# Kernel tuning notes

Hardware: AMD Instinct MI355X
Metric: run time of the kernel (lower is better)

The kernel has to match this reference:

```python
import jax, jax.numpy as jnp
import numpy as np

B, D, HID, DC, K = 32768, 64, 512, 128, 12
CLAMP = 1.0
L1 = D // 2          # GLOW split lengths
L2 = D - L1
INIT = 0.01          # torch code rescales all params to 0.01*randn


def setup_inputs() -> dict:
    key = jax.random.key(0)
    ks = iter(jax.random.split(key, 16))
    # FrEIA PermuteRandom: np.random.seed(k); np.random.permutation(D)
    perms = jnp.asarray(
        np.stack([np.random.RandomState(k).permutation(D) for k in range(K)]),
        dtype=jnp.int32)
    f32 = jnp.float32
    return {
        'q_feat': jax.random.normal(next(ks), (B, 1, D), f32),
        'H': jax.random.normal(next(ks), (B, DC), f32),
        'perms': perms,
        'an_logscale': INIT * jax.random.normal(next(ks), (K, D), f32),
        'an_bias': INIT * jax.random.normal(next(ks), (K, D), f32),
        's1_W1': INIT * jax.random.normal(next(ks), (K, HID, L1 + DC), f32),
        's1_b1': INIT * jax.random.normal(next(ks), (K, HID), f32),
        's1_W2': INIT * jax.random.normal(next(ks), (K, 2 * L2, HID), f32),
        's1_b2': INIT * jax.random.normal(next(ks), (K, 2 * L2), f32),
        's2_W1': INIT * jax.random.normal(next(ks), (K, HID, L2 + DC), f32),
        's2_b1': INIT * jax.random.normal(next(ks), (K, HID), f32),
        's2_W2': INIT * jax.random.normal(next(ks), (K, 2 * L1, HID), f32),
        's2_b2': INIT * jax.random.normal(next(ks), (K, 2 * L1), f32),
    }


def _mlp(x, W1, b1, W2, b2):
    # torch Linear: y = x @ W.T + b
    h = jax.nn.relu(x @ W1.T + b1)
    return h @ W2.T + b2


def _log_e(s):
    # FrEIA GLOW soft clamp: log e(s) = clamp * 0.636 * atan(s / clamp)
    return CLAMP * 0.636 * jnp.arctan(s / CLAMP)


def reference(q_feat, H, perms, an_logscale, an_bias,
              s1_W1, s1_b1, s1_W2, s1_b2,
              s2_W1, s2_b1, s2_W2, s2_b2):
    x = q_feat.reshape(q_feat.shape[0], -1)          # Flatten: (B,1,D)->(B,D)
    logj = jnp.zeros(x.shape[0], x.dtype)

    def block(carry, p):
        x, logj = carry
        perm, ls, bi, w11, b11, w12, b12, w21, b21, w22, b22 = p
        x = x[:, perm]                               # PermuteRandom (logdet 0)
        x = x * jnp.exp(ls) + bi                     # ActNorm
        logj = logj + jnp.sum(ls)
        x1, x2 = x[:, :L1], x[:, L1:]                # GLOW coupling
        r2 = _mlp(jnp.concatenate([x2, H], 1), w21, b21, w22, b22)
        le2 = _log_e(r2[:, :L1])
        y1 = jnp.exp(le2) * x1 + r2[:, L1:]
        r1 = _mlp(jnp.concatenate([y1, H], 1), w11, b11, w12, b12)
        le1 = _log_e(r1[:, :L2])
        y2 = jnp.exp(le1) * x2 + r1[:, L2:]
        logj = logj + jnp.sum(le1, axis=1) + jnp.sum(le2, axis=1)
        return (jnp.concatenate([y1, y2], 1), logj), None

    (z, logj), _ = jax.lax.scan(
        block, (x, logj),
        (perms, an_logscale, an_bias,
         s1_W1, s1_b1, s1_W2, s1_b2,
         s2_W1, s2_b1, s2_W2, s2_b2))
    return z, logj
```

## Files before the change

### kernel.cpp

```cpp
#include <hip/hip_runtime.h>
#include <hip/hip_bf16.h>
#include <math.h>

#define B_ROWS 32768

typedef __attribute__((ext_vector_type(8)))  short        s8v;
typedef __attribute__((ext_vector_type(4)))  float        f4v;
typedef __attribute__((ext_vector_type(2)))  unsigned int u2v;
typedef __attribute__((ext_vector_type(4)))  unsigned int u4v;

__device__ __forceinline__ short f2bf(float f){
  unsigned u = __builtin_bit_cast(unsigned, f);
  u = (u + 0x7fffu + ((u >> 16) & 1u)) >> 16;
  return (short)u;
}
__device__ __forceinline__ unsigned cpk(float a, float b){
  __hip_bfloat16_raw lo = (__hip_bfloat16_raw)__float2bfloat16(a);
  __hip_bfloat16_raw hi = (__hip_bfloat16_raw)__float2bfloat16(b);
  return (unsigned)lo.x | ((unsigned)hi.x << 16);
}
__device__ __forceinline__ float bf_lo(unsigned u){ return __builtin_bit_cast(float, u << 16); }
__device__ __forceinline__ float bf_hi(unsigned u){ return __builtin_bit_cast(float, u & 0xffff0000u); }

__device__ __forceinline__ float atan_f(float t){
  float a = fabsf(t);
  bool big = a > 1.0f;
  float u = big ? __builtin_amdgcn_rcpf(t) : t;
  float s = u * u;
  float p = fmaf(fmaf(fmaf(fmaf(s, 0.0208351f, -0.0851330f), s, 0.1801410f), s, -0.3302995f), s, 0.9998660f);
  p = u * p;
  float base = __builtin_copysignf(1.57079633f, t);
  return big ? base - p : p;
}

#define MFMA16(A,B,C) __builtin_amdgcn_mfma_f32_16x16x32_bf16((A),(B),(C),0,0,0)

typedef __attribute__((address_space(1))) const unsigned int gu32;
typedef __attribute__((address_space(3))) unsigned int lu32;
__device__ __forceinline__ void gl_lds16(const unsigned short* g, char* l){
  __builtin_amdgcn_global_load_lds((gu32*)(const void*)g, (lu32*)(void*)l, 16, 0, 0);
}

#define OXFT 0
#define XFT_S 68
#define OXHB 17408
#define XHB_S 40
#define OHB  22528
#define HB_S 72
#define OSL  31744
#define SL_S 68
#define OW1  40448
#define W1BUF 20480
#define OLJ  81408
#define SM_SZ 81664

#define WF_W2 1966080
#define W_TOTAL 2752512

__global__ void cvtw_frag(const float* __restrict__ s1w1, const float* __restrict__ s1w2,
                          const float* __restrict__ s2w1, const float* __restrict__ s2w2,
                          unsigned short* __restrict__ dst)
{
  long t = (long)blockIdx.x * blockDim.x + threadIdx.x;
  if (t >= W_TOTAL) return;
  float v;
  if (t < WF_W2){
    int m = (int)(t / 81920); int r = (int)(t - (long)m*81920);
    int c = r / 10240;  int r2 = r - c*10240;
    int tile = r2 >> 9; int r3 = r2 & 511;
    int lane = r3 >> 3; int e = r3 & 7;
    int rg = tile / 5,  kk = tile - rg*5;
    int l15 = lane & 15, lq = lane >> 4;
    int h  = c*64 + rg*16 + l15;
    int ki = kk*32 + lq*8 + e;
    const float* src = (m & 1) ? s1w1 : s2w1;
    v = src[(size_t)(m >> 1)*81920 + h*160 + ki];
  } else {
    long u = t - WF_W2;
    int m = (int)(u / 32768); int r = (int)(u - (long)m*32768);
    int g = r >> 9; int r3 = r & 511;
    int lane = r3 >> 3; int e = r3 & 7;
    int c = g >> 3, hs = (g >> 2) & 1, ot = g & 3;
    int l15 = lane & 15, lq = lane >> 4;
    int o = ot*16 + l15;
    int h = c*64 + hs*32 + lq*8 + e;
    const float* src = (m & 1) ? s1w2 : s2w2;
    v = src[(size_t)(m >> 1)*32768 + o*512 + h];
  }
  dst[t] = (unsigned short)f2bf(v);
}

__global__ __launch_bounds__(256, 2) void cinn_dma2(
    const float* __restrict__ q, const float* __restrict__ Hg,
    const int* __restrict__ perms,
    const float* __restrict__ ls_g, const float* __restrict__ bi_g,
    const float* __restrict__ s1b1, const float* __restrict__ s1b2,
    const float* __restrict__ s2b1, const float* __restrict__ s2b2,
    const unsigned short* __restrict__ wbf,
    float* __restrict__ outz, float* __restrict__ outlj)
{
  __shared__ __align__(16) char sm[SM_SZ];
  const int tid = threadIdx.x;
  const int rowbase = blockIdx.x * 64;
  const int lane = tid & 63, wave = tid >> 6;
  const int hw = wave >> 1, ng = wave & 1;
  const int l15 = lane & 15, lq = lane >> 4;

  float* XFT = (float*)(sm + OXFT);
  short* XHB = (short*)(sm + OXHB);
  short* HB  = (short*)(sm + OHB);
  float* LOGJ= (float*)(sm + OLJ);

  {
    int b = tid >> 2, j = tid & 3;
    const float* src = q + (size_t)(rowbase + b)*64 + j*16;
    #pragma unroll
    for (int i = 0; i < 4; ++i){
      f4v v = *(const f4v*)(src + 4*i);
      #pragma unroll
      for (int jj = 0; jj < 4; ++jj)
        XFT[(j*16 + 4*i + jj)*XFT_S + b] = v[jj];
    }
  }
  if (tid < 64) LOGJ[tid] = 0.f;
  __syncthreads();

  s8v hfr[2][4];
  #pragma unroll
  for (int nt = 0; nt < 2; ++nt){
    int b = rowbase + ng*32 + nt*16 + l15;
    #pragma unroll
    for (int kkh = 0; kkh < 4; ++kkh){
      const float* hp = Hg + (size_t)b*128 + kkh*32 + lq*8;
      f4v a = *(const f4v*)hp;
      f4v c = *(const f4v*)(hp + 4);
      u4v u = {cpk(a[0],a[1]), cpk(a[2],a[3]), cpk(c[0],c[1]), cpk(c[2],c[3])};
      hfr[nt][kkh] = __builtin_bit_cast(s8v, u);
    }
  }

  {
    const unsigned short* g = wbf + wave*2560 + lane*8;
    char* lb = sm + OW1 + wave*5120;
    #pragma unroll
    for (int k = 0; k < 5; ++k) gl_lds16(g + k*512, lb + k*1024);
  }

  for (int m = 0; m < 24; ++m){
    const int bp = m & 1;
    const unsigned short* w1sec = wbf + (size_t)m*81920;
    const unsigned short* w2sec = wbf + WF_W2 + (size_t)m*32768;
    const float* b1p = (bp ? s1b1 : s2b1) + (m >> 1)*512;
    const float* b2p = (bp ? s1b2 : s2b2) + (m >> 1)*64;

    if (!bp){
      int blk = m >> 1;
      int   pd = perms[blk*64 + lane];
      float e  = __expf(ls_g[blk*64 + lane]);
      float bi = bi_g[blk*64 + lane];
      int bg = wave;
      f4v v[4];
      #pragma unroll
      for (int i = 0; i < 4; ++i)
        v[i] = *(const f4v*)(XFT + pd*XFT_S + bg*16 + 4*i);
      __syncthreads();
      #pragma unroll
      for (int i = 0; i < 4; ++i){
        #pragma unroll
        for (int jj = 0; jj < 4; ++jj) v[i][jj] = fmaf(v[i][jj], e, bi);
        *(f4v*)(XFT + lane*XFT_S + bg*16 + 4*i) = v[i];
      }
      if (lane >= 32){
        #pragma unroll
        for (int i = 0; i < 4; ++i)
          #pragma unroll
          for (int jj = 0; jj < 4; ++jj)
            XHB[(bg*16 + 4*i + jj)*XHB_S + (lane - 32)] = f2bf(v[i][jj]);
      }
      __syncthreads();
    }

    s8v xk[2];
    #pragma unroll
    for (int nt = 0; nt < 2; ++nt)
      xk[nt] = *(const s8v*)(XHB + (ng*32 + nt*16 + l15)*XHB_S + lq*8);

    f4v b2v[4];
    if (hw == 0){
      #pragma unroll
      for (int ot = 0; ot < 4; ++ot)
        b2v[ot] = *(const f4v*)(b2p + ot*16 + lq*4);
    }

    f4v racc[4][2];
    #pragma unroll
    for (int ot = 0; ot < 4; ++ot)
      #pragma unroll
      for (int nt = 0; nt < 2; ++nt)
        racc[ot][nt] = (f4v){0.f,0.f,0.f,0.f};

    #pragma unroll
    for (int c = 0; c < 8; ++c){
      if (!(m == 23 && c == 7)){
        const unsigned short* gsec = (c < 7) ? w1sec : (w1sec + 81920);
        const int cn = (c < 7) ? c + 1 : 0;
        const unsigned short* g = gsec + cn*10240 + wave*2560 + lane*8;
        char* lb = sm + OW1 + ((c+1)&1)*W1BUF + wave*5120;
        #pragma unroll
        for (int k = 0; k < 5; ++k) gl_lds16(g + k*512, lb + k*1024);
      }
      s8v w2c[4];
      #pragma unroll
      for (int ot = 0; ot < 4; ++ot)
        w2c[ot] = *(const s8v*)(w2sec + (size_t)((c*2 + hw)*4 + ot)*512 + lane*8);
      f4v b1v0 = *(const f4v*)(b1p + c*64 + hw*32 + lq*4);
      f4v b1v1 = *(const f4v*)(b1p + c*64 + hw*32 + 16 + lq*4);

      const short* W1c = (const short*)(sm + OW1 + (c&1)*W1BUF);
      f4v acc[2][2];
      #pragma unroll
      for (int mt = 0; mt < 2; ++mt)
        #pragma unroll
        for (int nt = 0; nt < 2; ++nt) acc[mt][nt] = (f4v){0.f,0.f,0.f,0.f};
      #pragma unroll
      for (int kk = 0; kk < 5; ++kk){
        s8v a0 = *(const s8v*)(W1c + ((hw*2 + 0)*5 + kk)*512 + lane*8);
        s8v a1 = *(const s8v*)(W1c + ((hw*2 + 1)*5 + kk)*512 + lane*8);
        #pragma unroll
        for (int nt = 0; nt < 2; ++nt){
          s8v bb = (kk == 0) ? xk[nt] : hfr[nt][kk-1];
          acc[0][nt] = MFMA16(a0, bb, acc[0][nt]);
          acc[1][nt] = MFMA16(a1, bb, acc[1][nt]);
        }
      }
      #pragma unroll
      for (int mt = 0; mt < 2; ++mt){
        f4v bv = mt ? b1v1 : b1v0;
        #pragma unroll
        for (int nt = 0; nt < 2; ++nt){
          float h0 = fmaxf(acc[mt][nt][0] + bv[0], 0.f);
          float h1 = fmaxf(acc[mt][nt][1] + bv[1], 0.f);
          float h2 = fmaxf(acc[mt][nt][2] + bv[2], 0.f);
          float h3 = fmaxf(acc[mt][nt][3] + bv[3], 0.f);
          *(u2v*)(HB + (ng*32 + nt*16 + l15)*HB_S + hw*32 + mt*16 + lq*4) = (u2v){cpk(h0,h1), cpk(h2,h3)};
        }
      }
      #pragma unroll
      for (int nt = 0; nt < 2; ++nt){
        s8v bb = *(const s8v*)(HB + (ng*32 + nt*16 + l15)*HB_S + hw*32 + lq*8);
        #pragma unroll
        for (int ot = 0; ot < 4; ++ot)
          racc[ot][nt] = MFMA16(w2c[ot], bb, racc[ot][nt]);
      }
      __syncthreads();
    }

    {
      short* SL = (hw == 0) ? (short*)(sm + OSL) : (short*)(sm + OHB);
      #pragma unroll
      for (int ot = 0; ot < 4; ++ot)
        #pragma unroll
        for (int nt = 0; nt < 2; ++nt){
          float r0 = racc[ot][nt][0], r1 = racc[ot][nt][1];
          float r2 = racc[ot][nt][2], r3 = racc[ot][nt][3];
          if (hw == 0){ r0 += b2v[ot][0]; r1 += b2v[ot][1]; r2 += b2v[ot][2]; r3 += b2v[ot][3]; }
          *(u2v*)(SL + (ng*32 + nt*16 + l15)*SL_S + ot*16 + lq*4) = (u2v){cpk(r0,r1), cpk(r2,r3)};
        }
    }
    __syncthreads();

    {
      int b = tid & 63, og = tid >> 6;
      float le[8] = {0,0,0,0,0,0,0,0}, ra[8] = {0,0,0,0,0,0,0,0};
      #pragma unroll
      for (int ms = 0; ms < 2; ++ms){
        const short* SL = (ms == 0) ? (const short*)(sm + OSL) : (const short*)(sm + OHB);
        u2v L0 = *(const u2v*)(SL + b*SL_S + og*8);
        u2v L1 = *(const u2v*)(SL + b*SL_S + og*8 + 4);
        u2v R0 = *(const u2v*)(SL + b*SL_S + 32 + og*8);
        u2v R1 = *(const u2v*)(SL + b*SL_S + 32 + og*8 + 4);
        le[0]+=bf_lo(L0[0]); le[1]+=bf_hi(L0[0]); le[2]+=bf_lo(L0[1]); le[3]+=bf_hi(L0[1]);
        le[4]+=bf_lo(L1[0]); le[5]+=bf_hi(L1[0]); le[6]+=bf_lo(L1[1]); le[7]+=bf_hi(L1[1]);
        ra[0]+=bf_lo(R0[0]); ra[1]+=bf_hi(R0[0]); ra[2]+=bf_lo(R0[1]); ra[3]+=bf_hi(R0[1]);
        ra[4]+=bf_lo(R1[0]); ra[5]+=bf_hi(R1[0]); ra[6]+=bf_lo(R1[1]); ra[7]+=bf_hi(R1[1]);
      }
      float part = 0.f, y[8];
      #pragma unroll
      for (int j = 0; j < 8; ++j){
        float l = 0.636f * atan_f(le[j]);
        int d = bp*32 + og*8 + j;
        y[j] = __expf(l) * XFT[d*XFT_S + b] + ra[j];
        XFT[d*XFT_S + b] = y[j];
        part += l;
      }
      if (!bp){
        u4v u = {cpk(y[0],y[1]), cpk(y[2],y[3]), cpk(y[4],y[5]), cpk(y[6],y[7])};
        *(u4v*)(XHB + b*XHB_S + og*8) = u;
      }
      atomicAdd(&LOGJ[b], part);
    }
    __syncthreads();
  }

  {
    int b = tid >> 2, j = tid & 3;
    float* dst = outz + (size_t)(rowbase + b)*64 + j*16;
    #pragma unroll
    for (int i = 0; i < 4; ++i){
      f4v w;
      #pragma unroll
      for (int jj = 0; jj < 4; ++jj)
        w[jj] = XFT[(j*16 + 4*i + jj)*XFT_S + b];
      *(f4v*)(dst + 4*i) = w;
    }
  }
  if (tid < 64){
    float p = 0.f;
    #pragma unroll
    for (int k = 0; k < 12; ++k) p += ls_g[k*64 + tid];
    #pragma unroll
    for (int off = 1; off < 64; off <<= 1) p += __shfl_xor(p, off);
    outlj[rowbase + tid] = LOGJ[tid] + p;
  }
}

extern "C" void kernel_launch(void* const* d_in, const int* in_sizes, int n_in,
                              void* d_out, int out_size, void* d_ws, size_t ws_size,
                              hipStream_t stream)
{
  const float* q    = (const float*)d_in[0];
  const float* Hg   = (const float*)d_in[1];
  const int*   perms= (const int*)  d_in[2];
  const float* ls   = (const float*)d_in[3];
  const float* bi   = (const float*)d_in[4];
  const float* s1W1 = (const float*)d_in[5];
  const float* s1b1 = (const float*)d_in[6];
  const float* s1W2 = (const float*)d_in[7];
  const float* s1b2 = (const float*)d_in[8];
  const float* s2W1 = (const float*)d_in[9];
  const float* s2b1 = (const float*)d_in[10];
  const float* s2W2 = (const float*)d_in[11];
  const float* s2b2 = (const float*)d_in[12];
  float* outz  = (float*)d_out;
  float* outlj = outz + (size_t)B_ROWS * 64;

  unsigned short* wbf = (unsigned short*)d_ws;
  cvtw_frag<<<2688, 1024, 0, stream>>>(s1W1, s1W2, s2W1, s2W2, wbf);
  cinn_dma2<<<512, 256, 0, stream>>>(q, Hg, perms, ls, bi,
                                     s1b1, s1b2, s2b1, s2b2,
                                     wbf, outz, outlj);
}
```

Baseline: 273.1 us.

## Widen blocks to 16 waves over 128 rows with larger W1 chunks

The fused flow kernel moves from 256-thread blocks on 64 rows to 1024-thread blocks on 128 rows. Each W1 chunk now covers 128 hidden units (40 KB, double-buffered), and the second-layer partial sums are split four ways across hidden-unit quarters. The aim is to have each weight chunk streamed into LDS serve twice as many rows, halving weight traffic per row and the number of chunk iterations. In exchange, LDS use grows to about 160 KB per block, so only one block fits per CU (256 blocks total). The four-way partial-sum reduction also adds LDS traffic and reuses the spare W1 buffer as scratch.

```diff
diff --git a/kernel.cpp b/kernel.cpp
--- a/kernel.cpp
+++ b/kernel.cpp
@@ -42,17 +42,17 @@
 }
 
 #define OXFT 0
-#define XFT_S 68
-#define OXHB 17408
+#define XFT_S 132
+#define OXHB 33792
 #define XHB_S 40
-#define OHB  22528
-#define HB_S 72
-#define OSL  31744
+#define OHB  44032
+#define HB_S 136
+#define OW1  78848
+#define W1BUF 40960
+#define OLJ  160768
+#define SM_SZ 161280
 #define SL_S 68
-#define OW1  40448
-#define W1BUF 20480
-#define OLJ  81408
-#define SM_SZ 81664
+#define SLOT_B 17408
 
 #define WF_W2 1966080
 #define W_TOTAL 2752512
@@ -66,12 +66,12 @@
   float v;
   if (t < WF_W2){
     int m = (int)(t / 81920); int r = (int)(t - (long)m*81920);
-    int c = r / 10240;  int r2 = r - c*10240;
+    int c = r / 20480;  int r2 = r - c*20480;
     int tile = r2 >> 9; int r3 = r2 & 511;
     int lane = r3 >> 3; int e = r3 & 7;
     int rg = tile / 5,  kk = tile - rg*5;
     int l15 = lane & 15, lq = lane >> 4;
-    int h  = c*64 + rg*16 + l15;
+    int h  = c*128 + rg*16 + l15;
     int ki = kk*32 + lq*8 + e;
     const float* src = (m & 1) ? s1w1 : s2w1;
     v = src[(size_t)(m >> 1)*81920 + h*160 + ki];
@@ -80,17 +80,24 @@
     int m = (int)(u / 32768); int r = (int)(u - (long)m*32768);
     int g = r >> 9; int r3 = r & 511;
     int lane = r3 >> 3; int e = r3 & 7;
-    int c = g >> 3, hs = (g >> 2) & 1, ot = g & 3;
+    int c = g >> 4, hw = (g >> 2) & 3, ot = g & 3;
     int l15 = lane & 15, lq = lane >> 4;
     int o = ot*16 + l15;
-    int h = c*64 + hs*32 + lq*8 + e;
+    int h = c*128 + hw*32 + lq*8 + e;
     const float* src = (m & 1) ? s1w2 : s2w2;
     v = src[(size_t)(m >> 1)*32768 + o*512 + h];
   }
   dst[t] = (unsigned short)f2bf(v);
 }
 
-__global__ __launch_bounds__(256, 2) void cinn_dma2(
+__device__ __forceinline__ void dma_w1(const unsigned short* gsec, char* lb, int wave, int lane){
+  gl_lds16(gsec + (size_t)wave*512 + lane*8,        lb + wave*1024);
+  gl_lds16(gsec + (size_t)(wave+16)*512 + lane*8,   lb + (wave+16)*1024);
+  if (wave < 8)
+    gl_lds16(gsec + (size_t)(wave+32)*512 + lane*8, lb + (wave+32)*1024);
+}
+
+__global__ __launch_bounds__(1024, 4) void cinn_w16(
     const float* __restrict__ q, const float* __restrict__ Hg,
     const int* __restrict__ perms,
     const float* __restrict__ ls_g, const float* __restrict__ bi_g,
@@ -101,9 +108,9 @@
 {
   __shared__ __align__(16) char sm[SM_SZ];
   const int tid = threadIdx.x;
-  const int rowbase = blockIdx.x * 64;
+  const int rowbase = blockIdx.x * 128;
   const int lane = tid & 63, wave = tid >> 6;
-  const int hw = wave >> 1, ng = wave & 1;
+  const int ng = wave >> 2, hw = wave & 3;
   const int l15 = lane & 15, lq = lane >> 4;
 
   float* XFT = (float*)(sm + OXFT);
@@ -112,17 +119,17 @@
   float* LOGJ= (float*)(sm + OLJ);
 
   {
-    int b = tid >> 2, j = tid & 3;
-    const float* src = q + (size_t)(rowbase + b)*64 + j*16;
-    #pragma unroll
-    for (int i = 0; i < 4; ++i){
-      f4v v = *(const f4v*)(src + 4*i);
-      #pragma unroll
-      for (int jj = 0; jj < 4; ++jj)
-        XFT[(j*16 + 4*i + jj)*XFT_S + b] = v[jj];
-    }
-  }
-  if (tid < 64) LOGJ[tid] = 0.f;
+    int b = tid >> 3, j = tid & 7;
+    const float* src = q + (size_t)(rowbase + b)*64 + j*8;
+    f4v v0 = *(const f4v*)src;
+    f4v v1 = *(const f4v*)(src + 4);
+    #pragma unroll
+    for (int jj = 0; jj < 4; ++jj){
+      XFT[(j*8 + jj)*XFT_S + b]     = v0[jj];
+      XFT[(j*8 + 4 + jj)*XFT_S + b] = v1[jj];
+    }
+  }
+  if (tid < 128) LOGJ[tid] = 0.f;
   __syncthreads();
 
   s8v hfr[2][4];
@@ -139,12 +146,7 @@
     }
   }
 
-  {
-    const unsigned short* g = wbf + wave*2560 + lane*8;
-    char* lb = sm + OW1 + wave*5120;
-    #pragma unroll
-    for (int k = 0; k < 5; ++k) gl_lds16(g + k*512, lb + k*1024);
-  }
+  dma_w1(wbf, sm + OW1, wave, lane);
 
   for (int m = 0; m < 24; ++m){
     const int bp = m & 1;
@@ -159,23 +161,23 @@
       float e  = __expf(ls_g[blk*64 + lane]);
       float bi = bi_g[blk*64 + lane];
       int bg = wave;
-      f4v v[4];
-      #pragma unroll
-      for (int i = 0; i < 4; ++i)
-        v[i] = *(const f4v*)(XFT + pd*XFT_S + bg*16 + 4*i);
+      f4v v[2];
+      #pragma unroll
+      for (int i = 0; i < 2; ++i)
+        v[i] = *(const f4v*)(XFT + pd*XFT_S + bg*8 + 4*i);
       __syncthreads();
       #pragma unroll
-      for (int i = 0; i < 4; ++i){
+      for (int i = 0; i < 2; ++i){
         #pragma unroll
         for (int jj = 0; jj < 4; ++jj) v[i][jj] = fmaf(v[i][jj], e, bi);
-        *(f4v*)(XFT + lane*XFT_S + bg*16 + 4*i) = v[i];
+        *(f4v*)(XFT + lane*XFT_S + bg*8 + 4*i) = v[i];
       }
       if (lane >= 32){
         #pragma unroll
-        for (int i = 0; i < 4; ++i)
+        for (int i = 0; i < 2; ++i)
           #pragma unroll
           for (int jj = 0; jj < 4; ++jj)
-            XHB[(bg*16 + 4*i + jj)*XHB_S + (lane - 32)] = f2bf(v[i][jj]);
+            XHB[(bg*8 + 4*i + jj)*XHB_S + (lane - 32)] = f2bf(v[i][jj]);
       }
       __syncthreads();
     }
@@ -200,21 +202,17 @@
         racc[ot][nt] = (f4v){0.f,0.f,0.f,0.f};
 
     #pragma unroll
-    for (int c = 0; c < 8; ++c){
-      if (!(m == 23 && c == 7)){
-        const unsigned short* gsec = (c < 7) ? w1sec : (w1sec + 81920);
-        const int cn = (c < 7) ? c + 1 : 0;
-        const unsigned short* g = gsec + cn*10240 + wave*2560 + lane*8;
-        char* lb = sm + OW1 + ((c+1)&1)*W1BUF + wave*5120;
-        #pragma unroll
-        for (int k = 0; k < 5; ++k) gl_lds16(g + k*512, lb + k*1024);
+    for (int c = 0; c < 4; ++c){
+      if (!(m == 23 && c == 3)){
+        const unsigned short* gsec = (c < 3) ? (w1sec + (c+1)*20480) : (w1sec + 81920);
+        dma_w1(gsec, sm + OW1 + ((c+1)&1)*W1BUF, wave, lane);
       }
       s8v w2c[4];
       #pragma unroll
       for (int ot = 0; ot < 4; ++ot)
-        w2c[ot] = *(const s8v*)(w2sec + (size_t)((c*2 + hw)*4 + ot)*512 + lane*8);
-      f4v b1v0 = *(const f4v*)(b1p + c*64 + hw*32 + lq*4);
-      f4v b1v1 = *(const f4v*)(b1p + c*64 + hw*32 + 16 + lq*4);
+        w2c[ot] = *(const s8v*)(w2sec + (size_t)((c*4 + hw)*4 + ot)*512 + lane*8);
+      f4v b1v0 = *(const f4v*)(b1p + c*128 + hw*32 + lq*4);
+      f4v b1v1 = *(const f4v*)(b1p + c*128 + hw*32 + 16 + lq*4);
 
       const short* W1c = (const short*)(sm + OW1 + (c&1)*W1BUF);
       f4v acc[2][2];
@@ -256,7 +254,8 @@
     }
 
     {
-      short* SL = (hw == 0) ? (short*)(sm + OSL) : (short*)(sm + OHB);
+      short* SL = (hw < 2) ? (short*)(sm + OHB + hw*SLOT_B)
+                           : (short*)(sm + OW1 + W1BUF + (hw-2)*SLOT_B);
       #pragma unroll
       for (int ot = 0; ot < 4; ++ot)
         #pragma unroll
@@ -270,54 +269,49 @@
     __syncthreads();
 
     {
-      int b = tid & 63, og = tid >> 6;
-      float le[8] = {0,0,0,0,0,0,0,0}, ra[8] = {0,0,0,0,0,0,0,0};
-      #pragma unroll
-      for (int ms = 0; ms < 2; ++ms){
-        const short* SL = (ms == 0) ? (const short*)(sm + OSL) : (const short*)(sm + OHB);
-        u2v L0 = *(const u2v*)(SL + b*SL_S + og*8);
-        u2v L1 = *(const u2v*)(SL + b*SL_S + og*8 + 4);
-        u2v R0 = *(const u2v*)(SL + b*SL_S + 32 + og*8);
-        u2v R1 = *(const u2v*)(SL + b*SL_S + 32 + og*8 + 4);
-        le[0]+=bf_lo(L0[0]); le[1]+=bf_hi(L0[0]); le[2]+=bf_lo(L0[1]); le[3]+=bf_hi(L0[1]);
-        le[4]+=bf_lo(L1[0]); le[5]+=bf_hi(L1[0]); le[6]+=bf_lo(L1[1]); le[7]+=bf_hi(L1[1]);
-        ra[0]+=bf_lo(R0[0]); ra[1]+=bf_hi(R0[0]); ra[2]+=bf_lo(R0[1]); ra[3]+=bf_hi(R0[1]);
-        ra[4]+=bf_lo(R1[0]); ra[5]+=bf_hi(R1[0]); ra[6]+=bf_lo(R1[1]); ra[7]+=bf_hi(R1[1]);
-      }
-      float part = 0.f, y[8];
-      #pragma unroll
-      for (int j = 0; j < 8; ++j){
+      int b = tid & 127, dg = tid >> 7;
+      float le[4] = {0,0,0,0}, ra[4] = {0,0,0,0};
+      #pragma unroll
+      for (int ms = 0; ms < 4; ++ms){
+        const short* SL = (ms < 2) ? (const short*)(sm + OHB + ms*SLOT_B)
+                                   : (const short*)(sm + OW1 + W1BUF + (ms-2)*SLOT_B);
+        u2v L = *(const u2v*)(SL + b*SL_S + dg*4);
+        u2v R = *(const u2v*)(SL + b*SL_S + 32 + dg*4);
+        le[0]+=bf_lo(L[0]); le[1]+=bf_hi(L[0]); le[2]+=bf_lo(L[1]); le[3]+=bf_hi(L[1]);
+        ra[0]+=bf_lo(R[0]); ra[1]+=bf_hi(R[0]); ra[2]+=bf_lo(R[1]); ra[3]+=bf_hi(R[1]);
+      }
+      float part = 0.f, y[4];
+      #pragma unroll
+      for (int j = 0; j < 4; ++j){
         float l = 0.636f * atan_f(le[j]);
-        int d = bp*32 + og*8 + j;
+        int d = bp*32 + dg*4 + j;
         y[j] = __expf(l) * XFT[d*XFT_S + b] + ra[j];
         XFT[d*XFT_S + b] = y[j];
         part += l;
       }
-      if (!bp){
-        u4v u = {cpk(y[0],y[1]), cpk(y[2],y[3]), cpk(y[4],y[5]), cpk(y[6],y[7])};
-        *(u4v*)(XHB + b*XHB_S + og*8) = u;
-      }
+      if (!bp)
+        *(u2v*)(XHB + b*XHB_S + dg*4) = (u2v){cpk(y[0],y[1]), cpk(y[2],y[3])};
       atomicAdd(&LOGJ[b], part);
     }
     __syncthreads();
   }
 
   {
-    int b = tid >> 2, j = tid & 3;
-    float* dst = outz + (size_t)(rowbase + b)*64 + j*16;
-    #pragma unroll
-    for (int i = 0; i < 4; ++i){
-      f4v w;
-      #pragma unroll
-      for (int jj = 0; jj < 4; ++jj)
-        w[jj] = XFT[(j*16 + 4*i + jj)*XFT_S + b];
-      *(f4v*)(dst + 4*i) = w;
-    }
-  }
-  if (tid < 64){
+    int b = tid >> 3, j = tid & 7;
+    float* dst = outz + (size_t)(rowbase + b)*64 + j*8;
+    f4v w0, w1;
+    #pragma unroll
+    for (int jj = 0; jj < 4; ++jj){
+      w0[jj] = XFT[(j*8 + jj)*XFT_S + b];
+      w1[jj] = XFT[(j*8 + 4 + jj)*XFT_S + b];
+    }
+    *(f4v*)dst = w0;
+    *(f4v*)(dst + 4) = w1;
+  }
+  if (tid < 128){
     float p = 0.f;
     #pragma unroll
-    for (int k = 0; k < 12; ++k) p += ls_g[k*64 + tid];
+    for (int k = 0; k < 12; ++k) p += ls_g[k*64 + lane];
     #pragma unroll
     for (int off = 1; off < 64; off <<= 1) p += __shfl_xor(p, off);
     outlj[rowbase + tid] = LOGJ[tid] + p;
@@ -346,7 +340,7 @@
 
   unsigned short* wbf = (unsigned short*)d_ws;
   cvtw_frag<<<2688, 1024, 0, stream>>>(s1W1, s1W2, s2W1, s2W2, wbf);
-  cinn_dma2<<<512, 256, 0, stream>>>(q, Hg, perms, ls, bi,
+  cinn_w16<<<256, 1024, 0, stream>>>(q, Hg, perms, ls, bi,
                                      s1b1, s1b2, s2b1, s2b2,
                                      wbf, outz, outlj);
 }
```

Result: slower. 484.0 us (+77.2%).

## Double row tile to 128 per block with 512 threads and wider hidden chunks

Applied to the files above, without the earlier changes.

The main kernel now handles 128 rows per block with 8 waves and 1 block per CU instead of 64 rows with 4 waves. Hidden units are processed in 4 chunks of 128, so each weight tile staged into LDS is reused across twice as many rows and the per-row weight traffic roughly halves. Bias adds are folded into the accumulator initialisation. The weight conversion kernel is rewritten to read 8 contiguous floats per thread and store packed 16-byte values in the same fragment layout. LDS use roughly doubles to about 160KB, so only one block fits per CU, which risks less latency hiding and only 256 blocks on the grid.

```diff
diff --git a/kernel.cpp b/kernel.cpp
--- a/kernel.cpp
+++ b/kernel.cpp
@@ -42,55 +42,55 @@
 }
 
 #define OXFT 0
-#define XFT_S 68
-#define OXHB 17408
+#define XFT_S 132
+#define OXHB 33792
 #define XHB_S 40
-#define OHB  22528
-#define HB_S 72
-#define OSL  31744
+#define OHB  44032
+#define HB_S 136
+#define OW1  78848
+#define W1BUF 40960
+#define OLJ  160768
+#define SM_SZ 161280
 #define SL_S 68
-#define OW1  40448
-#define W1BUF 20480
-#define OLJ  81408
-#define SM_SZ 81664
+#define SLOT_B 17408
 
 #define WF_W2 1966080
 #define W_TOTAL 2752512
 
-__global__ void cvtw_frag(const float* __restrict__ s1w1, const float* __restrict__ s1w2,
-                          const float* __restrict__ s2w1, const float* __restrict__ s2w2,
-                          unsigned short* __restrict__ dst)
+#define NT_W1 245760
+#define NT_W2 98304
+__global__ void cvtw_lin(const float* __restrict__ s1w1, const float* __restrict__ s1w2,
+                         const float* __restrict__ s2w1, const float* __restrict__ s2w2,
+                         unsigned short* __restrict__ dst)
 {
-  long t = (long)blockIdx.x * blockDim.x + threadIdx.x;
-  if (t >= W_TOTAL) return;
-  float v;
-  if (t < WF_W2){
-    int m = (int)(t / 81920); int r = (int)(t - (long)m*81920);
-    int c = r / 10240;  int r2 = r - c*10240;
-    int tile = r2 >> 9; int r3 = r2 & 511;
-    int lane = r3 >> 3; int e = r3 & 7;
-    int rg = tile / 5,  kk = tile - rg*5;
-    int l15 = lane & 15, lq = lane >> 4;
-    int h  = c*64 + rg*16 + l15;
-    int ki = kk*32 + lq*8 + e;
-    const float* src = (m & 1) ? s1w1 : s2w1;
-    v = src[(size_t)(m >> 1)*81920 + h*160 + ki];
-  } else {
-    long u = t - WF_W2;
-    int m = (int)(u / 32768); int r = (int)(u - (long)m*32768);
-    int g = r >> 9; int r3 = r & 511;
-    int lane = r3 >> 3; int e = r3 & 7;
-    int c = g >> 3, hs = (g >> 2) & 1, ot = g & 3;
-    int l15 = lane & 15, lq = lane >> 4;
-    int o = ot*16 + l15;
-    int h = c*64 + hs*32 + lq*8 + e;
-    const float* src = (m & 1) ? s1w2 : s2w2;
-    v = src[(size_t)(m >> 1)*32768 + o*512 + h];
-  }
-  dst[t] = (unsigned short)f2bf(v);
-}
-
-__global__ __launch_bounds__(256, 2) void cinn_dma2(
+  int t = blockIdx.x * blockDim.x + threadIdx.x;
+  if (t < NT_W1){
+    int lqkk = t % 20;  int u2 = t / 20;
+    int h = u2 & 127;   int mc = u2 >> 7;
+    int c = mc & 3,  m = mc >> 2;
+    int kk = lqkk >> 2, lq = lqkk & 3;
+    int rg = h >> 4, l15 = h & 15;
+    const float* src = ((m & 1) ? s1w1 : s2w1) + (size_t)(m >> 1)*81920
+                       + (size_t)(c*128 + h)*160 + lqkk*8;
+    f4v a = *(const f4v*)src;
+    f4v b = *(const f4v*)(src + 4);
+    u4v o = {cpk(a[0],a[1]), cpk(a[2],a[3]), cpk(b[0],b[1]), cpk(b[2],b[3])};
+    *(u4v*)(dst + (size_t)m*81920 + c*20480 + (rg*5 + kk)*512 + (lq*16 + l15)*8) = o;
+  } else if (t < NT_W1 + NT_W2){
+    int v = t - NT_W1;
+    int chl = v & 63;  int u2 = v >> 6;
+    int ol = u2 & 63;  int m = u2 >> 6;
+    int c = chl >> 4, hw = (chl >> 2) & 3, lq = chl & 3;
+    int ot = ol >> 4, l15 = ol & 15;
+    const float* src = ((m & 1) ? s1w2 : s2w2) + (size_t)(m >> 1)*32768 + (ot*16 + l15)*512 + chl*8;
+    f4v a = *(const f4v*)src;
+    f4v b = *(const f4v*)(src + 4);
+    u4v o = {cpk(a[0],a[1]), cpk(a[2],a[3]), cpk(b[0],b[1]), cpk(b[2],b[3])};
+    *(u4v*)(dst + WF_W2 + (size_t)m*32768 + ((c*4 + hw)*4 + ot)*512 + (lq*16 + l15)*8) = o;
+  }
+}
+
+__global__ __launch_bounds__(512, 1) void cinn_dma(
     const float* __restrict__ q, const float* __restrict__ Hg,
     const int* __restrict__ perms,
     const float* __restrict__ ls_g, const float* __restrict__ bi_g,
@@ -101,7 +101,7 @@
 {
   __shared__ __align__(16) char sm[SM_SZ];
   const int tid = threadIdx.x;
-  const int rowbase = blockIdx.x * 64;
+  const int rowbase = blockIdx.x * 128;
   const int lane = tid & 63, wave = tid >> 6;
   const int hw = wave >> 1, ng = wave & 1;
   const int l15 = lane & 15, lq = lane >> 4;
@@ -122,13 +122,13 @@
         XFT[(j*16 + 4*i + jj)*XFT_S + b] = v[jj];
     }
   }
-  if (tid < 64) LOGJ[tid] = 0.f;
+  if (tid < 128) LOGJ[tid] = 0.f;
   __syncthreads();
 
-  s8v hfr[2][4];
+  s8v hfr[4][4];
   #pragma unroll
-  for (int nt = 0; nt < 2; ++nt){
-    int b = rowbase + ng*32 + nt*16 + l15;
+  for (int nt = 0; nt < 4; ++nt){
+    int b = rowbase + ng*64 + nt*16 + l15;
     #pragma unroll
     for (int kkh = 0; kkh < 4; ++kkh){
       const float* hp = Hg + (size_t)b*128 + kkh*32 + lq*8;
@@ -180,74 +180,66 @@
       __syncthreads();
     }
 
-    s8v xk[2];
-    #pragma unroll
-    for (int nt = 0; nt < 2; ++nt)
-      xk[nt] = *(const s8v*)(XHB + (ng*32 + nt*16 + l15)*XHB_S + lq*8);
-
-    f4v b2v[4];
-    if (hw == 0){
+    s8v xk[4];
+    #pragma unroll
+    for (int nt = 0; nt < 4; ++nt)
+      xk[nt] = *(const s8v*)(XHB + (ng*64 + nt*16 + l15)*XHB_S + lq*8);
+
+    f4v racc[4][4];
+    #pragma unroll
+    for (int ot = 0; ot < 4; ++ot){
+      f4v bv = (f4v){0.f,0.f,0.f,0.f};
+      if (hw == 0) bv = *(const f4v*)(b2p + ot*16 + lq*4);
+      #pragma unroll
+      for (int nt = 0; nt < 4; ++nt) racc[ot][nt] = bv;
+    }
+
+    #pragma unroll
+    for (int c = 0; c < 4; ++c){
+      if (!(m == 23 && c == 3)){
+        const unsigned short* gsec = (c < 3) ? (w1sec + (c+1)*20480) : (w1sec + 81920);
+        const unsigned short* g = gsec + wave*2560 + lane*8;
+        char* lb = sm + OW1 + ((c+1)&1)*W1BUF + wave*5120;
+        #pragma unroll
+        for (int k = 0; k < 5; ++k) gl_lds16(g + k*512, lb + k*1024);
+      }
+      s8v w2c[4];
       #pragma unroll
       for (int ot = 0; ot < 4; ++ot)
-        b2v[ot] = *(const f4v*)(b2p + ot*16 + lq*4);
-    }
-
-    f4v racc[4][2];
-    #pragma unroll
-    for (int ot = 0; ot < 4; ++ot)
-      #pragma unroll
-      for (int nt = 0; nt < 2; ++nt)
-        racc[ot][nt] = (f4v){0.f,0.f,0.f,0.f};
-
-    #pragma unroll
-    for (int c = 0; c < 8; ++c){
-      if (!(m == 23 && c == 7)){
-        const unsigned short* gsec = (c < 7) ? w1sec : (w1sec + 81920);
-        const int cn = (c < 7) ? c + 1 : 0;
-        const unsigned short* g = gsec + cn*10240 + wave*2560 + lane*8;
-        char* lb = sm + OW1 + ((c+1)&1)*W1BUF + wave*5120;
-        #pragma unroll
-        for (int k = 0; k < 5; ++k) gl_lds16(g + k*512, lb + k*1024);
-      }
-      s8v w2c[4];
-      #pragma unroll
-      for (int ot = 0; ot < 4; ++ot)
-        w2c[ot] = *(const s8v*)(w2sec + (size_t)((c*2 + hw)*4 + ot)*512 + lane*8);
-      f4v b1v0 = *(const f4v*)(b1p + c*64 + hw*32 + lq*4);
-      f4v b1v1 = *(const f4v*)(b1p + c*64 + hw*32 + 16 + lq*4);
+        w2c[ot] = *(const s8v*)(w2sec + (size_t)((c*4 + hw)*4 + ot)*512 + lane*8);
 
       const short* W1c = (const short*)(sm + OW1 + (c&1)*W1BUF);
-      f4v acc[2][2];
-      #pragma unroll
-      for (int mt = 0; mt < 2; ++mt)
-        #pragma unroll
-        for (int nt = 0; nt < 2; ++nt) acc[mt][nt] = (f4v){0.f,0.f,0.f,0.f};
+      f4v acc[2][4];
+      {
+        f4v b1v0 = *(const f4v*)(b1p + c*128 + hw*32 + lq*4);
+        f4v b1v1 = *(const f4v*)(b1p + c*128 + hw*32 + 16 + lq*4);
+        #pragma unroll
+        for (int nt = 0; nt < 4; ++nt){ acc[0][nt] = b1v0; acc[1][nt] = b1v1; }
+      }
       #pragma unroll
       for (int kk = 0; kk < 5; ++kk){
         s8v a0 = *(const s8v*)(W1c + ((hw*2 + 0)*5 + kk)*512 + lane*8);
         s8v a1 = *(const s8v*)(W1c + ((hw*2 + 1)*5 + kk)*512 + lane*8);
         #pragma unroll
-        for (int nt = 0; nt < 2; ++nt){
+        for (int nt = 0; nt < 4; ++nt){
           s8v bb = (kk == 0) ? xk[nt] : hfr[nt][kk-1];
           acc[0][nt] = MFMA16(a0, bb, acc[0][nt]);
           acc[1][nt] = MFMA16(a1, bb, acc[1][nt]);
         }
       }
       #pragma unroll
-      for (int mt = 0; mt < 2; ++mt){
-        f4v bv = mt ? b1v1 : b1v0;
-        #pragma unroll
-        for (int nt = 0; nt < 2; ++nt){
-          float h0 = fmaxf(acc[mt][nt][0] + bv[0], 0.f);
-          float h1 = fmaxf(acc[mt][nt][1] + bv[1], 0.f);
-          float h2 = fmaxf(acc[mt][nt][2] + bv[2], 0.f);
-          float h3 = fmaxf(acc[mt][nt][3] + bv[3], 0.f);
-          *(u2v*)(HB + (ng*32 + nt*16 + l15)*HB_S + hw*32 + mt*16 + lq*4) = (u2v){cpk(h0,h1), cpk(h2,h3)};
+      for (int mt = 0; mt < 2; ++mt)
+        #pragma unroll
+        for (int nt = 0; nt < 4; ++nt){
+          float h0 = fmaxf(acc[mt][nt][0], 0.f);
+          float h1 = fmaxf(acc[mt][nt][1], 0.f);
+          float h2 = fmaxf(acc[mt][nt][2], 0.f);
+          float h3 = fmaxf(acc[mt][nt][3], 0.f);
+          *(u2v*)(HB + (ng*64 + nt*16 + l15)*HB_S + hw*32 + mt*16 + lq*4) = (u2v){cpk(h0,h1), cpk(h2,h3)};
         }
-      }
-      #pragma unroll
-      for (int nt = 0; nt < 2; ++nt){
-        s8v bb = *(const s8v*)(HB + (ng*32 + nt*16 + l15)*HB_S + hw*32 + lq*8);
+      #pragma unroll
+      for (int nt = 0; nt < 4; ++nt){
+        s8v bb = *(const s8v*)(HB + (ng*64 + nt*16 + l15)*HB_S + hw*32 + lq*8);
         #pragma unroll
         for (int ot = 0; ot < 4; ++ot)
           racc[ot][nt] = MFMA16(w2c[ot], bb, racc[ot][nt]);
@@ -256,25 +248,24 @@
     }
 
     {
-      short* SL = (hw == 0) ? (short*)(sm + OSL) : (short*)(sm + OHB);
+      short* SL = (hw < 2) ? (short*)(sm + OHB + hw*SLOT_B)
+                           : (short*)(sm + OW1 + W1BUF + (hw-2)*SLOT_B);
       #pragma unroll
       for (int ot = 0; ot < 4; ++ot)
         #pragma unroll
-        for (int nt = 0; nt < 2; ++nt){
-          float r0 = racc[ot][nt][0], r1 = racc[ot][nt][1];
-          float r2 = racc[ot][nt][2], r3 = racc[ot][nt][3];
-          if (hw == 0){ r0 += b2v[ot][0]; r1 += b2v[ot][1]; r2 += b2v[ot][2]; r3 += b2v[ot][3]; }
-          *(u2v*)(SL + (ng*32 + nt*16 + l15)*SL_S + ot*16 + lq*4) = (u2v){cpk(r0,r1), cpk(r2,r3)};
-        }
+        for (int nt = 0; nt < 4; ++nt)
+          *(u2v*)(SL + (ng*64 + nt*16 + l15)*SL_S + ot*16 + lq*4) =
+            (u2v){cpk(racc[ot][nt][0], racc[ot][nt][1]), cpk(racc[ot][nt][2], racc[ot][nt][3])};
     }
     __syncthreads();
 
     {
-      int b = tid & 63, og = tid >> 6;
+      int b = tid & 127, og = tid >> 7;
       float le[8] = {0,0,0,0,0,0,0,0}, ra[8] = {0,0,0,0,0,0,0,0};
       #pragma unroll
-      for (int ms = 0; ms < 2; ++ms){
-        const short* SL = (ms == 0) ? (const short*)(sm + OSL) : (const short*)(sm + OHB);
+      for (int ms = 0; ms < 4; ++ms){
+        const short* SL = (ms < 2) ? (const short*)(sm + OHB + ms*SLOT_B)
+                                   : (const short*)(sm + OW1 + W1BUF + (ms-2)*SLOT_B);
         u2v L0 = *(const u2v*)(SL + b*SL_S + og*8);
         u2v L1 = *(const u2v*)(SL + b*SL_S + og*8 + 4);
         u2v R0 = *(const u2v*)(SL + b*SL_S + 32 + og*8);
@@ -293,10 +284,8 @@
         XFT[d*XFT_S + b] = y[j];
         part += l;
       }
-      if (!bp){
-        u4v u = {cpk(y[0],y[1]), cpk(y[2],y[3]), cpk(y[4],y[5]), cpk(y[6],y[7])};
-        *(u4v*)(XHB + b*XHB_S + og*8) = u;
-      }
+      if (!bp)
+        *(u4v*)(XHB + b*XHB_S + og*8) = (u4v){cpk(y[0],y[1]), cpk(y[2],y[3]), cpk(y[4],y[5]), cpk(y[6],y[7])};
       atomicAdd(&LOGJ[b], part);
     }
     __syncthreads();
@@ -314,10 +303,10 @@
       *(f4v*)(dst + 4*i) = w;
     }
   }
-  if (tid < 64){
+  if (tid < 128){
     float p = 0.f;
     #pragma unroll
-    for (int k = 0; k < 12; ++k) p += ls_g[k*64 + tid];
+    for (int k = 0; k < 12; ++k) p += ls_g[k*64 + lane];
     #pragma unroll
     for (int off = 1; off < 64; off <<= 1) p += __shfl_xor(p, off);
     outlj[rowbase + tid] = LOGJ[tid] + p;
@@ -345,8 +334,8 @@
   float* outlj = outz + (size_t)B_ROWS * 64;
 
   unsigned short* wbf = (unsigned short*)d_ws;
-  cvtw_frag<<<2688, 1024, 0, stream>>>(s1W1, s1W2, s2W1, s2W2, wbf);
-  cinn_dma2<<<512, 256, 0, stream>>>(q, Hg, perms, ls, bi,
-                                     s1b1, s1b2, s2b1, s2b2,
-                                     wbf, outz, outlj);
-}
+  cvtw_lin<<<1344, 256, 0, stream>>>(s1W1, s1W2, s2W1, s2W2, wbf);
+  cinn_dma<<<256, 512, 0, stream>>>(q, Hg, perms, ls, bi,
+                                    s1b1, s1b2, s2b1, s2b2,
+                                    wbf, outz, outlj);
+}
```

Measured after the change: 264.5 us. -3.2%, faster.
